# Optimization experiments

Hardware: AMD Instinct MI355X
Metric: run time of the kernel (lower is better)

The kernel has to match this reference:

```python
import jax, jax.numpy as jnp
import numpy as np

VOCAB = 50000
EMB = 100
HID = 128
NPROD = 10000
PEMB = 50
B, T = 256, 512
IN = EMB + PEMB  # 150


def setup_inputs() -> dict:
    key = jax.random.key(0)
    ks = jax.random.split(key, 10)
    s = 1.0 / np.sqrt(HID)  # torch LSTM init scale
    emb = jax.random.normal(ks[0], (VOCAB, EMB), jnp.float32)
    emb = emb.at[0].set(0.0)  # padding_idx=0
    return {
        "review": jax.random.randint(ks[1], (B, T), 0, VOCAB),
        "product": jax.random.randint(ks[2], (B,), 0, NPROD),
        "embedding": emb,
        "product_embedding": jax.random.normal(ks[3], (NPROD, PEMB), jnp.float32),
        "W_ih": jax.random.uniform(ks[4], (4 * HID, IN), jnp.float32, -s, s),
        "W_hh": jax.random.uniform(ks[5], (4 * HID, HID), jnp.float32, -s, s),
        "b_ih": jax.random.uniform(ks[6], (4 * HID,), jnp.float32, -s, s),
        "b_hh": jax.random.uniform(ks[7], (4 * HID,), jnp.float32, -s, s),
        "fc_w": jax.random.uniform(ks[8], (1, HID), jnp.float32, -s, s),
        "fc_b": jax.random.uniform(ks[9], (1,), jnp.float32, -s, s),
    }


def _lstm_last_h(x_proj, W_hh):
    # x_proj: [T, B, 4H] = precomputed input projection + biases
    def step(carry, xg):
        h, c = carry
        gates = xg + h @ W_hh.T  # [B, 4H]
        i, f, g, o = jnp.split(gates, 4, axis=-1)  # torch gate order i,f,g,o
        i, f, o = jax.nn.sigmoid(i), jax.nn.sigmoid(f), jax.nn.sigmoid(o)
        g = jnp.tanh(g)
        c = f * c + i * g
        h = o * jnp.tanh(c)
        return (h, c), None

    b = x_proj.shape[1]
    init = (jnp.zeros((b, HID), x_proj.dtype), jnp.zeros((b, HID), x_proj.dtype))
    (h, _), _ = jax.lax.scan(step, init, x_proj)
    return h  # [B, H] — hidden state at last timestep


def reference(review, product, embedding, product_embedding, W_ih, W_hh, b_ih, b_hh, fc_w, fc_b):
    er = embedding[review]                       # [B, T, EMB]
    ep = product_embedding[product][:, None, :]  # [B, 1, PEMB]
    ep = jnp.broadcast_to(ep, (er.shape[0], er.shape[1], PEMB))
    combined = jnp.concatenate([er, ep], axis=-1)  # [B, T, IN]
    # precompute input projection for all timesteps in one GEMM
    x_proj = jnp.einsum('btd,gd->tbg', combined, W_ih) + (b_ih + b_hh)  # [T, B, 4H]
    h_last = _lstm_last_h(x_proj, W_hh)
    out = h_last @ fc_w.T + fc_b  # [B, 1]
    return jax.nn.sigmoid(out)
```

## Files before the change

kernel.cpp:

```cpp
#include <hip/hip_runtime.h>
#include <hip/hip_bf16.h>
#include <math.h>

#define VOCAB 50000
#define EMB 100
#define HID 128
#define NPROD 10000
#define PEMB 50
#define BSZ 256
#define TLEN 512
#define INDIM 150
#define G4 512

typedef __attribute__((ext_vector_type(4))) float f32x4;

__device__ __forceinline__ float sigm(float x) {
    return __builtin_amdgcn_rcpf(1.f + __expf(-x));
}
__device__ __forceinline__ float tanh_fast(float x) {
    float e = __expf(-2.f * fabsf(x));
    float r = (1.f - e) * __builtin_amdgcn_rcpf(1.f + e);
    return __builtin_copysignf(r, x);
}

__global__ void k_transpose(const float* __restrict__ W_ih, float* __restrict__ Wt) {
    int idx = blockIdx.x * blockDim.x + threadIdx.x;
    if (idx < INDIM * G4) {
        int d = idx / G4, g = idx % G4;
        Wt[idx] = W_ih[g * INDIM + d];
    }
}

__global__ void k_pbias(const int* __restrict__ product,
                        const float* __restrict__ pemb,
                        const float* __restrict__ Wt,
                        const float* __restrict__ b_ih,
                        const float* __restrict__ b_hh,
                        float* __restrict__ pbias) {
    __shared__ float ep_s[PEMB];
    int b = blockIdx.x;
    int tid = threadIdx.x;
    int p = product[b];
    if (tid < PEMB) ep_s[tid] = pemb[p * PEMB + tid];
    __syncthreads();
    int g0 = tid, g1 = tid + 256;
    float a0 = b_ih[g0] + b_hh[g0];
    float a1 = b_ih[g1] + b_hh[g1];
    #pragma unroll 5
    for (int d = 0; d < PEMB; ++d) {
        float e = ep_s[d];
        a0 += e * Wt[(EMB + d) * G4 + g0];
        a1 += e * Wt[(EMB + d) * G4 + g1];
    }
    pbias[b * G4 + g0] = a0;
    pbias[b * G4 + g1] = a1;
}

__global__ void k_table(const float* __restrict__ emb,
                        const float* __restrict__ Wt,
                        float* __restrict__ table) {
    __shared__ __align__(16) float es[16 * EMB];
    int v0 = blockIdx.x * 16;
    int tid = threadIdx.x;
    for (int l = tid; l < 16 * EMB; l += 256) es[l] = emb[v0 * EMB + l];
    __syncthreads();
    float acc0[16], acc1[16];
    #pragma unroll
    for (int r = 0; r < 16; ++r) { acc0[r] = 0.f; acc1[r] = 0.f; }
    #pragma unroll 5
    for (int k4 = 0; k4 < EMB / 4; ++k4) {
        float w0[4], w1[4];
        #pragma unroll
        for (int j = 0; j < 4; ++j) {
            w0[j] = Wt[(k4 * 4 + j) * G4 + tid];
            w1[j] = Wt[(k4 * 4 + j) * G4 + tid + 256];
        }
        #pragma unroll
        for (int r = 0; r < 16; ++r) {
            float4 e = *reinterpret_cast<const float4*>(&es[r * EMB + k4 * 4]);
            acc0[r] += e.x * w0[0] + e.y * w0[1] + e.z * w0[2] + e.w * w0[3];
            acc1[r] += e.x * w1[0] + e.y * w1[1] + e.z * w1[2] + e.w * w1[3];
        }
    }
    #pragma unroll
    for (int r = 0; r < 16; ++r) {
        table[(v0 + r) * G4 + tid]       = acc0[r];
        table[(v0 + r) * G4 + tid + 256] = acc1[r];
    }
}

__global__ void
__attribute__((amdgpu_flat_work_group_size(512, 512), amdgpu_waves_per_eu(2, 2)))
k_lstm(
    const int* __restrict__ review,
    const float* __restrict__ W_hh,
    const float* __restrict__ table,
    const float* __restrict__ pbias,
    const float* __restrict__ fc_w,
    const float* __restrict__ fc_b,
    float* __restrict__ out) {
    __shared__ __align__(16) float hsA[HID];
    __shared__ __align__(16) float hsB[HID];
    __shared__ float gsh[G4];
    __shared__ int rv_s[TLEN];
    int b = blockIdx.x;
    int g = threadIdx.x;
    int wgate = g >> 7;
    int u = g & 127;

    rv_s[g] = review[b * TLEN + g];
    if (g < HID) { hsA[g] = 0.f; hsB[g] = 0.f; }
    __syncthreads();

    float x_cur = table[rv_s[0] * G4 + g];
    float pb = pbias[b * G4 + g];

    float w[128];
    #pragma unroll
    for (int j = 0; j < 32; ++j) {
        f32x4 t = *reinterpret_cast<const f32x4*>(W_hh + g * HID + 4 * j);
        w[4 * j + 0] = t.x; w[4 * j + 1] = t.y; w[4 * j + 2] = t.z; w[4 * j + 3] = t.w;
    }
    #pragma unroll
    for (int k = 0; k < 128; ++k) asm volatile("" : "+v"(w[k]));

    const float* hr = hsA;
    float* hw = hsB;
    float c = 0.f;

    for (int t = 0; t < TLEN; ++t) {
        float x_next = table[rv_s[(t + 1) & (TLEN - 1)] * G4 + g];

        float a0 = 0.f, a1 = 0.f, a2 = 0.f, a3 = 0.f;
        #pragma unroll
        for (int j = 0; j < 32; ++j) {
            f32x4 h4 = *reinterpret_cast<const f32x4*>(&hr[4 * j]);
            a0 += h4.x * w[4 * j + 0];
            a1 += h4.y * w[4 * j + 1];
            a2 += h4.z * w[4 * j + 2];
            a3 += h4.w * w[4 * j + 3];
        }
        float pre = x_cur + pb + ((a0 + a1) + (a2 + a3));
        float act = (wgate == 2) ? tanh_fast(pre) : sigm(pre);
        gsh[g] = act;
        __syncthreads();

        float gi = gsh[u];
        float gf = gsh[HID + u];
        float gg = gsh[2 * HID + u];
        float go = gsh[3 * HID + u];
        c = gf * c + gi * gg;
        float h = go * tanh_fast(c);
        if (g < HID) hw[g] = h;
        __syncthreads();

        const float* tmp = hr; hr = hw; hw = (float*)tmp;
        x_cur = x_next;
    }

    if (g < 64) {
        float v = hr[g] * fc_w[g] + hr[g + 64] * fc_w[g + 64];
        #pragma unroll
        for (int off = 32; off >= 1; off >>= 1) v += __shfl_xor(v, off);
        if (g == 0) out[b] = sigm(v + fc_b[0]);
    }
}

extern "C" void kernel_launch(void* const* d_in, const int* in_sizes, int n_in,
                              void* d_out, int out_size, void* d_ws, size_t ws_size,
                              hipStream_t stream) {
    const int*   review  = (const int*)d_in[0];
    const int*   product = (const int*)d_in[1];
    const float* emb     = (const float*)d_in[2];
    const float* pemb    = (const float*)d_in[3];
    const float* W_ih    = (const float*)d_in[4];
    const float* W_hh    = (const float*)d_in[5];
    const float* b_ih    = (const float*)d_in[6];
    const float* b_hh    = (const float*)d_in[7];
    const float* fc_w    = (const float*)d_in[8];
    const float* fc_b    = (const float*)d_in[9];
    float* out = (float*)d_out;

    char* ws = (char*)d_ws;
    float* Wt    = (float*)(ws);
    float* pbias = (float*)(ws + 307200);
    float* table = (float*)(ws + 831488);

    k_transpose<<<(INDIM * G4 + 255) / 256, 256, 0, stream>>>(W_ih, Wt);
    k_pbias<<<BSZ, 256, 0, stream>>>(product, pemb, Wt, b_ih, b_hh, pbias);
    k_table<<<VOCAB / 16, 256, 0, stream>>>(emb, Wt, table);
    k_lstm<<<BSZ, 512, 0, stream>>>(review, W_hh, table, pbias, fc_w, fc_b, out);
}
```

Before: 643.3 us.

## Batch 16 sequences per block and compute recurrence with split-bf16 MFMA

The LSTM recurrence now handles 16 batch rows per workgroup (16 blocks instead of 256). It computes h@W_hh^T with bf16 MFMA 16x16x32, using a hi/lo split of weights and hidden state to recover near-fp32 precision. Gate columns are permuted so each lane holds i,f,g,o for its unit, which removes the gate-exchange barrier and leaves one sync per step. The aim is to trade per-row scalar FMAs for matrix instructions, at the cost of using only 16 CUs and three MFMA passes per step.

```diff
diff --git a/kernel.cpp b/kernel.cpp
--- a/kernel.cpp
+++ b/kernel.cpp
@@ -11,8 +11,12 @@
 #define TLEN 512
 #define INDIM 150
 #define G4 512
+#define RPB 16
+#define NBLK (BSZ/RPB)
 
 typedef __attribute__((ext_vector_type(4))) float f32x4;
+typedef __attribute__((ext_vector_type(8))) short short8;
+typedef __attribute__((ext_vector_type(4))) short short4v;
 
 __device__ __forceinline__ float sigm(float x) {
     return __builtin_amdgcn_rcpf(1.f + __expf(-x));
@@ -22,12 +26,21 @@
     float r = (1.f - e) * __builtin_amdgcn_rcpf(1.f + e);
     return __builtin_copysignf(r, x);
 }
+__device__ __forceinline__ short f2bf(float f) {
+    __hip_bfloat16 h = __float2bfloat16(f);
+    return __builtin_bit_cast(short, h);
+}
+__device__ __forceinline__ float bf2f(short s) {
+    __hip_bfloat16 h = __builtin_bit_cast(__hip_bfloat16, s);
+    return __bfloat162float(h);
+}
+__device__ __forceinline__ int jperm(int j) { return ((j & 3) << 7) + (j >> 2); }
 
 __global__ void k_transpose(const float* __restrict__ W_ih, float* __restrict__ Wt) {
     int idx = blockIdx.x * blockDim.x + threadIdx.x;
     if (idx < INDIM * G4) {
-        int d = idx / G4, g = idx % G4;
-        Wt[idx] = W_ih[g * INDIM + d];
+        int d = idx / G4, j = idx % G4;
+        Wt[idx] = W_ih[jperm(j) * INDIM + d];
     }
 }
 
@@ -43,17 +56,18 @@
     int p = product[b];
     if (tid < PEMB) ep_s[tid] = pemb[p * PEMB + tid];
     __syncthreads();
-    int g0 = tid, g1 = tid + 256;
+    int j0 = tid, j1 = tid + 256;
+    int g0 = jperm(j0), g1 = jperm(j1);
     float a0 = b_ih[g0] + b_hh[g0];
     float a1 = b_ih[g1] + b_hh[g1];
     #pragma unroll 5
     for (int d = 0; d < PEMB; ++d) {
         float e = ep_s[d];
-        a0 += e * Wt[(EMB + d) * G4 + g0];
-        a1 += e * Wt[(EMB + d) * G4 + g1];
-    }
-    pbias[b * G4 + g0] = a0;
-    pbias[b * G4 + g1] = a1;
+        a0 += e * Wt[(EMB + d) * G4 + j0];
+        a1 += e * Wt[(EMB + d) * G4 + j1];
+    }
+    pbias[b * G4 + j0] = a0;
+    pbias[b * G4 + j1] = a1;
 }
 
 __global__ void k_table(const float* __restrict__ emb,
@@ -91,78 +105,154 @@
 
 __global__ void
 __attribute__((amdgpu_flat_work_group_size(512, 512), amdgpu_waves_per_eu(2, 2)))
-k_lstm(
-    const int* __restrict__ review,
-    const float* __restrict__ W_hh,
-    const float* __restrict__ table,
-    const float* __restrict__ pbias,
-    const float* __restrict__ fc_w,
-    const float* __restrict__ fc_b,
-    float* __restrict__ out) {
-    __shared__ __align__(16) float hsA[HID];
-    __shared__ __align__(16) float hsB[HID];
-    __shared__ float gsh[G4];
-    __shared__ int rv_s[TLEN];
-    int b = blockIdx.x;
-    int g = threadIdx.x;
-    int wgate = g >> 7;
-    int u = g & 127;
-
-    rv_s[g] = review[b * TLEN + g];
-    if (g < HID) { hsA[g] = 0.f; hsB[g] = 0.f; }
+k_lstm(const int* __restrict__ review,
+       const float* __restrict__ W_hh,
+       const float* __restrict__ table,
+       const float* __restrict__ pbias,
+       const float* __restrict__ fc_w,
+       const float* __restrict__ fc_b,
+       float* __restrict__ out) {
+    __shared__ int rv_s[RPB][TLEN + 1];
+    __shared__ short hbuf[2][2][RPB * HID];
+
+    const int tid = threadIdx.x;
+    const int w   = tid >> 6;
+    const int l   = tid & 63;
+    const int row = l & 15;
+    const int lk  = l >> 4;
+    const int b0  = blockIdx.x * RPB;
+
+    #pragma unroll 1
+    for (int r = 0; r < RPB; ++r)
+        rv_s[r][tid] = review[(b0 + r) * TLEN + tid];
+    {
+        int4 z = {0, 0, 0, 0};
+        int4* hz = (int4*)hbuf;
+        hz[tid] = z; hz[tid + 512] = z;
+    }
+
+    short8 ahi[4][4], alo[4][4];
+    #pragma unroll
+    for (int jt = 0; jt < 4; ++jt) {
+        #pragma unroll
+        for (int kt = 0; kt < 4; ++kt) {
+            int j = (w << 6) + (jt << 4) + row;
+            int g = jperm(j);
+            const float* wr = W_hh + g * HID + (kt << 5) + (lk << 3);
+            float4 wa = *reinterpret_cast<const float4*>(wr);
+            float4 wb = *reinterpret_cast<const float4*>(wr + 4);
+            float wf[8] = {wa.x, wa.y, wa.z, wa.w, wb.x, wb.y, wb.z, wb.w};
+            short8 h8, l8;
+            #pragma unroll
+            for (int q = 0; q < 8; ++q) {
+                short hq = f2bf(wf[q]);
+                h8[q] = hq;
+                l8[q] = f2bf(wf[q] - bf2f(hq));
+            }
+            ahi[jt][kt] = h8; alo[jt][kt] = l8;
+        }
+    }
+
+    float4 pb[4];
+    #pragma unroll
+    for (int jt = 0; jt < 4; ++jt)
+        pb[jt] = *reinterpret_cast<const float4*>(
+            pbias + (b0 + row) * G4 + (w << 6) + (jt << 4) + (lk << 2));
+
     __syncthreads();
 
-    float x_cur = table[rv_s[0] * G4 + g];
-    float pb = pbias[b * G4 + g];
-
-    float w[128];
-    #pragma unroll
-    for (int j = 0; j < 32; ++j) {
-        f32x4 t = *reinterpret_cast<const f32x4*>(W_hh + g * HID + 4 * j);
-        w[4 * j + 0] = t.x; w[4 * j + 1] = t.y; w[4 * j + 2] = t.z; w[4 * j + 3] = t.w;
-    }
-    #pragma unroll
-    for (int k = 0; k < 128; ++k) asm volatile("" : "+v"(w[k]));
-
-    const float* hr = hsA;
-    float* hw = hsB;
-    float c = 0.f;
-
+    float4 xc[4];
+    {
+        int v = rv_s[row][0];
+        const float* xr = table + (long)v * G4 + (w << 6) + (lk << 2);
+        #pragma unroll
+        for (int jt = 0; jt < 4; ++jt) xc[jt] = *reinterpret_cast<const float4*>(xr + (jt << 4));
+    }
+
+    float cst[4] = {0.f, 0.f, 0.f, 0.f};
+    int p = 0;
+    const int rb = row << 8;
+    const int sw = (row & 7) << 4;
+
+    #pragma unroll 1
     for (int t = 0; t < TLEN; ++t) {
-        float x_next = table[rv_s[(t + 1) & (TLEN - 1)] * G4 + g];
-
-        float a0 = 0.f, a1 = 0.f, a2 = 0.f, a3 = 0.f;
-        #pragma unroll
-        for (int j = 0; j < 32; ++j) {
-            f32x4 h4 = *reinterpret_cast<const f32x4*>(&hr[4 * j]);
-            a0 += h4.x * w[4 * j + 0];
-            a1 += h4.y * w[4 * j + 1];
-            a2 += h4.z * w[4 * j + 2];
-            a3 += h4.w * w[4 * j + 3];
-        }
-        float pre = x_cur + pb + ((a0 + a1) + (a2 + a3));
-        float act = (wgate == 2) ? tanh_fast(pre) : sigm(pre);
-        gsh[g] = act;
+        float4 xn[4];
+        {
+            int v = rv_s[row][(t + 1) & (TLEN - 1)];
+            const float* xr = table + (long)v * G4 + (w << 6) + (lk << 2);
+            #pragma unroll
+            for (int jt = 0; jt < 4; ++jt) xn[jt] = *reinterpret_cast<const float4*>(xr + (jt << 4));
+        }
+
+        const char* hhi_p = (const char*)hbuf[p][0];
+        const char* hlo_p = (const char*)hbuf[p][1];
+
+        f32x4 z4 = {0.f, 0.f, 0.f, 0.f};
+        f32x4 acc[4] = {z4, z4, z4, z4};
+        short8 bh[4];
+        #pragma unroll
+        for (int kt = 0; kt < 4; ++kt) {
+            int byte = (rb + (kt << 6) + (lk << 4)) ^ sw;
+            bh[kt] = *reinterpret_cast<const short8*>(hhi_p + byte);
+        }
+        #pragma unroll
+        for (int jt = 0; jt < 4; ++jt) {
+            #pragma unroll
+            for (int kt = 0; kt < 4; ++kt) {
+                acc[jt] = __builtin_amdgcn_mfma_f32_16x16x32_bf16(ahi[jt][kt], bh[kt], acc[jt], 0, 0, 0);
+                acc[jt] = __builtin_amdgcn_mfma_f32_16x16x32_bf16(alo[jt][kt], bh[kt], acc[jt], 0, 0, 0);
+            }
+        }
+        #pragma unroll
+        for (int kt = 0; kt < 4; ++kt) {
+            int byte = (rb + (kt << 6) + (lk << 4)) ^ sw;
+            bh[kt] = *reinterpret_cast<const short8*>(hlo_p + byte);
+        }
+        #pragma unroll
+        for (int jt = 0; jt < 4; ++jt) {
+            #pragma unroll
+            for (int kt = 0; kt < 4; ++kt)
+                acc[jt] = __builtin_amdgcn_mfma_f32_16x16x32_bf16(ahi[jt][kt], bh[kt], acc[jt], 0, 0, 0);
+        }
+
+        char* whi = (char*)hbuf[p ^ 1][0];
+        char* wlo = (char*)hbuf[p ^ 1][1];
+        #pragma unroll
+        for (int jt = 0; jt < 4; ++jt) {
+            float p0 = acc[jt][0] + xc[jt].x + pb[jt].x;
+            float p1 = acc[jt][1] + xc[jt].y + pb[jt].y;
+            float p2 = acc[jt][2] + xc[jt].z + pb[jt].z;
+            float p3 = acc[jt][3] + xc[jt].w + pb[jt].w;
+            float gi = sigm(p0), gf = sigm(p1), gg = tanh_fast(p2), go = sigm(p3);
+            cst[jt] = gf * cst[jt] + gi * gg;
+            float h = go * tanh_fast(cst[jt]);
+            short hh = f2bf(h);
+            short hl = f2bf(h - bf2f(hh));
+            int unit = (w << 4) + (jt << 2) + lk;
+            int byte = (rb + (unit << 1)) ^ sw;
+            *reinterpret_cast<short*>(whi + byte) = hh;
+            *reinterpret_cast<short*>(wlo + byte) = hl;
+        }
         __syncthreads();
-
-        float gi = gsh[u];
-        float gf = gsh[HID + u];
-        float gg = gsh[2 * HID + u];
-        float go = gsh[3 * HID + u];
-        c = gf * c + gi * gg;
-        float h = go * tanh_fast(c);
-        if (g < HID) hw[g] = h;
-        __syncthreads();
-
-        const float* tmp = hr; hr = hw; hw = (float*)tmp;
-        x_cur = x_next;
-    }
-
-    if (g < 64) {
-        float v = hr[g] * fc_w[g] + hr[g + 64] * fc_w[g + 64];
-        #pragma unroll
-        for (int off = 32; off >= 1; off >>= 1) v += __shfl_xor(v, off);
-        if (g == 0) out[b] = sigm(v + fc_b[0]);
+        p ^= 1;
+        #pragma unroll
+        for (int jt = 0; jt < 4; ++jt) xc[jt] = xn[jt];
+    }
+
+    {
+        const char* fhi = (const char*)hbuf[p][0];
+        const char* flo = (const char*)hbuf[p][1];
+        int r = tid >> 5, seg = tid & 31;
+        int byte = ((r << 8) + (seg << 3)) ^ ((r & 7) << 4);
+        short4v h4 = *reinterpret_cast<const short4v*>(fhi + byte);
+        short4v l4 = *reinterpret_cast<const short4v*>(flo + byte);
+        float s = 0.f;
+        #pragma unroll
+        for (int q = 0; q < 4; ++q)
+            s += (bf2f(h4[q]) + bf2f(l4[q])) * fc_w[(seg << 2) + q];
+        #pragma unroll
+        for (int off = 16; off >= 1; off >>= 1) s += __shfl_xor(s, off);
+        if (seg == 0) out[b0 + r] = sigm(s + fc_b[0]);
     }
 }
 
@@ -189,5 +279,5 @@
     k_transpose<<<(INDIM * G4 + 255) / 256, 256, 0, stream>>>(W_ih, Wt);
     k_pbias<<<BSZ, 256, 0, stream>>>(product, pemb, Wt, b_ih, b_hh, pbias);
     k_table<<<VOCAB / 16, 256, 0, stream>>>(emb, Wt, table);
-    k_lstm<<<BSZ, 512, 0, stream>>>(review, W_hh, table, pbias, fc_w, fc_b, out);
-}
+    k_lstm<<<NBLK, 512, 0, stream>>>(review, W_hh, table, pbias, fc_w, fc_b, out);
+}
```

After: 1.037 ms. 1.61x slower.
